# Kernel tuning notes

Hardware: AMD Instinct MI355X
Metric: run time of the kernel (lower is better)

The kernel has to match this reference:

```python
import jax, jax.numpy as jnp
import numpy as np

N = 100000      # nodes
E = 3200000     # directed edges (avg degree 32)
F_IN = 512      # data.num_features
H = 64          # hidden_channels
C = 8           # data.num_classes


def setup_inputs() -> dict:
    key = jax.random.key(0)
    k = jax.random.split(key, 5)
    x = jax.random.normal(k[0], (N, F_IN), dtype=jnp.float32)
    edge_index = jax.random.randint(k[1], (2, E), 0, N, dtype=jnp.int32)
    W1 = jax.random.normal(k[2], (F_IN, H), dtype=jnp.float32) * (1.0 / np.sqrt(F_IN))
    b1 = jnp.zeros((H,), dtype=jnp.float32)
    W2 = jax.random.normal(k[3], (H, C), dtype=jnp.float32) * (1.0 / np.sqrt(H))
    b2 = jnp.zeros((C,), dtype=jnp.float32)
    return {"x": x, "edge_index": edge_index, "W1": W1, "b1": b1, "W2": W2, "b2": b2}


def _gcn_conv(x, W, b, src, dst, n):
    # PyG GCNConv: transform first, then aggregate with symmetric normalization.
    h = x @ W  # [N, out]
    ones = jnp.ones(src.shape[0], dtype=h.dtype)
    deg = jax.ops.segment_sum(ones, dst, num_segments=n)          # in-degree incl. self-loop
    dinv = jnp.where(deg > 0, jax.lax.rsqrt(deg), 0.0)
    norm = dinv[src] * dinv[dst]                                   # [E+N]
    out = jax.ops.segment_sum(h[src] * norm[:, None], dst, num_segments=n)
    return out + b


def reference(x, edge_index, W1, b1, W2, b2):
    # add self-loops once (gcn_norm adds them inside each GCNConv)
    loops = jnp.arange(N, dtype=edge_index.dtype)
    src = jnp.concatenate([edge_index[0], loops])
    dst = jnp.concatenate([edge_index[1], loops])
    h = jax.nn.relu(_gcn_conv(x, W1, b1, src, dst, N))
    # F.dropout(training=False) -> identity in eval mode
    return _gcn_conv(h, W2, b2, src, dst, N)
```

## Files before the change

kernel.cpp:

```cpp
#include <hip/hip_runtime.h>
#include <cstdint>
#include <cstddef>


#define NODE_SHIFT 7
#define NODE_RANGE 128
#define MAX_B 1024
#define CHUNK 16384

__device__ __forceinline__ unsigned short f2bf(float f) {
    unsigned u = __float_as_uint(f);
    u += 0x7FFFu + ((u >> 16) & 1u);
    return (unsigned short)(u >> 16);
}
__device__ __forceinline__ float bf2f(unsigned short h) {
    return __uint_as_float((unsigned)h << 16);
}

__global__ void k_zero(int* __restrict__ p, int n) {
    int i = blockIdx.x * blockDim.x + threadIdx.x;
    if (i < n) p[i] = 0;
}

__global__ __launch_bounds__(256) void k_bcount(const int* __restrict__ dst,
                                                int* __restrict__ bucket_cnt,
                                                int* __restrict__ blk_base,
                                                int E, int B) {
    __shared__ int hist[MAX_B];
    int t = threadIdx.x;
    for (int i = t; i < B; i += 256) hist[i] = 0;
    __syncthreads();
    int base = blockIdx.x * CHUNK;
#pragma unroll 8
    for (int j = 0; j < CHUNK / 256; ++j) {
        int e = base + j * 256 + t;
        if (e < E) atomicAdd(&hist[dst[e] >> NODE_SHIFT], 1);
    }
    __syncthreads();
    for (int i = t; i < B; i += 256)
        blk_base[(size_t)blockIdx.x * B + i] = atomicAdd(&bucket_cnt[i], hist[i]);
}

__global__ __launch_bounds__(1024) void k_bscan(const int* __restrict__ bucket_cnt,
                                                int* __restrict__ bucket_start,
                                                int* __restrict__ rowptr,
                                                int B, int N) {
    __shared__ int s[1024];
    int t = threadIdx.x;
    int v = (t < B) ? bucket_cnt[t] : 0;
    s[t] = v;
    __syncthreads();
    for (int off = 1; off < 1024; off <<= 1) {
        int add = (t >= off) ? s[t - off] : 0;
        __syncthreads();
        s[t] += add;
        __syncthreads();
    }
    if (t < B) bucket_start[t] = s[t] - v;
    if (t == 1023) {
        bucket_start[B] = s[1023];
        rowptr[N] = s[1023];
    }
}

__global__ __launch_bounds__(256) void k_bscatter(const int* __restrict__ src,
                                                  const int* __restrict__ dst,
                                                  const int* __restrict__ bucket_start,
                                                  const int* __restrict__ blk_base,
                                                  unsigned* __restrict__ bucket_pk,
                                                  int E, int B) {
    __shared__ int cur[MAX_B];
    int t = threadIdx.x;
    for (int i = t; i < B; i += 256)
        cur[i] = bucket_start[i] + blk_base[(size_t)blockIdx.x * B + i];
    __syncthreads();
    int base = blockIdx.x * CHUNK;
#pragma unroll 8
    for (int j = 0; j < CHUNK / 256; ++j) {
        int e = base + j * 256 + t;
        if (e < E) {
            int d = dst[e];
            int p = atomicAdd(&cur[d >> NODE_SHIFT], 1);
            bucket_pk[p] = (unsigned)src[e] | ((unsigned)(d & (NODE_RANGE - 1)) << 25);
        }
    }
}

__global__ __launch_bounds__(256) void k_bfinal(const unsigned* __restrict__ bucket_pk,
                                                const int* __restrict__ bucket_start,
                                                int* __restrict__ rowptr,
                                                float* __restrict__ dinv,
                                                int* __restrict__ csr_src,
                                                int N) {
    __shared__ int hist[NODE_RANGE];
    __shared__ int sc[NODE_RANGE];
    int t = threadIdx.x;
    int node0 = blockIdx.x * NODE_RANGE;
    int nn = min(NODE_RANGE, N - node0);
    int estart = bucket_start[blockIdx.x];
    int eend   = bucket_start[blockIdx.x + 1];

    if (t < NODE_RANGE) hist[t] = 0;
    __syncthreads();
    for (int e = estart + t; e < eend; e += 256)
        atomicAdd(&hist[bucket_pk[e] >> 25], 1);
    __syncthreads();

    int v = 0;
    if (t < NODE_RANGE) { v = hist[t]; sc[t] = v; }
    __syncthreads();
    for (int off = 1; off < NODE_RANGE; off <<= 1) {
        int add = (t < NODE_RANGE && t >= off) ? sc[t - off] : 0;
        __syncthreads();
        if (t < NODE_RANGE) sc[t] += add;
        __syncthreads();
    }

    int excl = (t < NODE_RANGE) ? (sc[t] - v) : 0;
    if (t < NODE_RANGE) hist[t] = estart + excl;
    if (t < nn) {
        rowptr[node0 + t] = estart + excl;
        dinv[node0 + t] = rsqrtf((float)(v + 1));
    }
    __syncthreads();

    for (int e = estart + t; e < eend; e += 256) {
        unsigned q = bucket_pk[e];
        int slot = atomicAdd(&hist[q >> 25], 1);
        csr_src[slot] = (int)(q & 0x01FFFFFFu);
    }
}


__global__ __launch_bounds__(256) void k_gemm1(const float* __restrict__ x,
                                               const float* __restrict__ W1,
                                               unsigned short* __restrict__ h1,
                                               int N) {
    __shared__ float xsT[32][68];
    __shared__ float ws[32][64];
    int t = threadIdx.x;
    int tc = t & 15;
    int tr = t >> 4;
    int row0 = blockIdx.x * 64;

    float acc[4][4] = {{0.f}};

    int lr  = t >> 2;
    int lkq = (t & 3) * 8;

    for (int k0 = 0; k0 < 512; k0 += 32) {
        {
            int gr = row0 + lr;
            float4 v0 = {0.f, 0.f, 0.f, 0.f}, v1 = {0.f, 0.f, 0.f, 0.f};
            if (gr < N) {
                const float* p = x + (size_t)gr * 512 + k0 + lkq;
                v0 = *(const float4*)p;
                v1 = *(const float4*)(p + 4);
            }
            xsT[lkq + 0][lr] = v0.x; xsT[lkq + 1][lr] = v0.y;
            xsT[lkq + 2][lr] = v0.z; xsT[lkq + 3][lr] = v0.w;
            xsT[lkq + 4][lr] = v1.x; xsT[lkq + 5][lr] = v1.y;
            xsT[lkq + 6][lr] = v1.z; xsT[lkq + 7][lr] = v1.w;
        }
        {
            const float* p = W1 + (size_t)k0 * 64 + t * 8;
            float4 v0 = *(const float4*)p;
            float4 v1 = *(const float4*)(p + 4);
            int kk = (t * 8) >> 6;
            int cc = (t * 8) & 63;
            *(float4*)&ws[kk][cc]     = v0;
            *(float4*)&ws[kk][cc + 4] = v1;
        }
        __syncthreads();

#pragma unroll
        for (int kk = 0; kk < 32; ++kk) {
            float4 a = *(const float4*)&xsT[kk][tr * 4];
            float4 b = *(const float4*)&ws[kk][tc * 4];
            acc[0][0] += a.x * b.x; acc[0][1] += a.x * b.y;
            acc[0][2] += a.x * b.z; acc[0][3] += a.x * b.w;
            acc[1][0] += a.y * b.x; acc[1][1] += a.y * b.y;
            acc[1][2] += a.y * b.z; acc[1][3] += a.y * b.w;
            acc[2][0] += a.z * b.x; acc[2][1] += a.z * b.y;
            acc[2][2] += a.z * b.z; acc[2][3] += a.z * b.w;
            acc[3][0] += a.w * b.x; acc[3][1] += a.w * b.y;
            acc[3][2] += a.w * b.z; acc[3][3] += a.w * b.w;
        }
        __syncthreads();
    }

#pragma unroll
    for (int r = 0; r < 4; ++r) {
        int gr = row0 + tr * 4 + r;
        if (gr < N) {
            ushort4 o;
            o.x = f2bf(acc[r][0]); o.y = f2bf(acc[r][1]);
            o.z = f2bf(acc[r][2]); o.w = f2bf(acc[r][3]);
            *(ushort4*)&h1[(size_t)gr * 64 + tc * 4] = o;
        }
    }
}


__global__ __launch_bounds__(256) void k_agg1(const unsigned short* __restrict__ h1,
                                              const int* __restrict__ rowptr,
                                              const int* __restrict__ csr_src,
                                              const float* __restrict__ dinv,
                                              const float* __restrict__ b1,
                                              const float* __restrict__ W2,
                                              float* __restrict__ h2, int N) {
    int wid = threadIdx.x >> 6;
    int lane = threadIdx.x & 63;
    int n = blockIdx.x * 4 + wid;
    if (n >= N) return;

    float w2r[8];
#pragma unroll
    for (int c = 0; c < 8; ++c) w2r[c] = W2[lane * 8 + c];
    float bias = b1[lane];
    float dn   = dinv[n];
    float self = bf2f(h1[(size_t)n * 64 + lane]);

    int start = __builtin_amdgcn_readfirstlane(rowptr[n]);
    int cnt   = __builtin_amdgcn_readfirstlane(rowptr[n + 1]) - start;
    const int* qp = csr_src + start;

    float acc0 = 0.f, acc1 = 0.f;
    int i = 0;
    for (; i + 8 <= cnt; i += 8) {
        int q0 = qp[i + 0]; int q1 = qp[i + 1];
        int q2 = qp[i + 2]; int q3 = qp[i + 3];
        int q4 = qp[i + 4]; int q5 = qp[i + 5];
        int q6 = qp[i + 6]; int q7 = qp[i + 7];
        float w0 = dinv[q0]; float w1 = dinv[q1];
        float w2 = dinv[q2]; float w3 = dinv[q3];
        float w4 = dinv[q4]; float w5 = dinv[q5];
        float w6 = dinv[q6]; float w7 = dinv[q7];
        float v0 = bf2f(h1[(size_t)q0 * 64 + lane]);
        float v1 = bf2f(h1[(size_t)q1 * 64 + lane]);
        float v2 = bf2f(h1[(size_t)q2 * 64 + lane]);
        float v3 = bf2f(h1[(size_t)q3 * 64 + lane]);
        float v4 = bf2f(h1[(size_t)q4 * 64 + lane]);
        float v5 = bf2f(h1[(size_t)q5 * 64 + lane]);
        float v6 = bf2f(h1[(size_t)q6 * 64 + lane]);
        float v7 = bf2f(h1[(size_t)q7 * 64 + lane]);
        acc0 = fmaf(w0, v0, acc0);
        acc1 = fmaf(w1, v1, acc1);
        acc0 = fmaf(w2, v2, acc0);
        acc1 = fmaf(w3, v3, acc1);
        acc0 = fmaf(w4, v4, acc0);
        acc1 = fmaf(w5, v5, acc1);
        acc0 = fmaf(w6, v6, acc0);
        acc1 = fmaf(w7, v7, acc1);
    }
    for (; i < cnt; ++i) {
        int q = qp[i];
        acc0 = fmaf(dinv[q], bf2f(h1[(size_t)q * 64 + lane]), acc0);
    }

    float r = fmaxf(dn * ((acc0 + acc1) + dn * self) + bias, 0.f);

    float keep = 0.f;
#pragma unroll
    for (int c = 0; c < 8; ++c) {
        float s = r * w2r[c];
#pragma unroll
        for (int k = 1; k < 64; k <<= 1) s += __shfl_xor(s, k, 64);
        keep = ((lane & 7) == c) ? s : keep;
    }
    if (lane < 8) h2[(size_t)n * 8 + lane] = keep;
}


__global__ __launch_bounds__(256) void k_agg2(const float* __restrict__ h2,
                                              const int* __restrict__ rowptr,
                                              const int* __restrict__ csr_src,
                                              const float* __restrict__ dinv,
                                              const float* __restrict__ b2,
                                              float* __restrict__ out, int N) {
    int wid = threadIdx.x >> 6;
    int lane = threadIdx.x & 63;
    int n = blockIdx.x * 4 + wid;
    if (n >= N) return;
    int start = rowptr[n];
    int cnt = rowptr[n + 1] - start;
    int c = lane & 7;
    int ii = lane >> 3;

    float a0 = 0.f, a1 = 0.f;
    int i = ii;
    for (; i + 8 < cnt; i += 16) {
        int q0 = csr_src[start + i];
        int q1 = csr_src[start + i + 8];
        float w0 = dinv[q0], w1 = dinv[q1];
        float v0 = h2[(size_t)q0 * 8 + c];
        float v1 = h2[(size_t)q1 * 8 + c];
        a0 = fmaf(w0, v0, a0);
        a1 = fmaf(w1, v1, a1);
    }
    if (i < cnt) {
        int q = csr_src[start + i];
        a0 = fmaf(dinv[q], h2[(size_t)q * 8 + c], a0);
    }
    float acc = a0 + a1;
    acc += __shfl_xor(acc, 8, 64);
    acc += __shfl_xor(acc, 16, 64);
    acc += __shfl_xor(acc, 32, 64);

    if (lane < 8) {
        float dn = dinv[n];
        out[(size_t)n * 8 + lane] =
            dn * (acc + dn * h2[(size_t)n * 8 + lane]) + b2[lane];
    }
}


extern "C" void kernel_launch(void* const* d_in, const int* in_sizes, int n_in,
                              void* d_out, int out_size, void* d_ws, size_t ws_size,
                              hipStream_t stream) {
    const float* x  = (const float*)d_in[0];
    const int*   ei = (const int*)d_in[1];
    const float* W1 = (const float*)d_in[2];
    const float* b1 = (const float*)d_in[3];
    const float* W2 = (const float*)d_in[4];
    const float* b2 = (const float*)d_in[5];
    float* out = (float*)d_out;

    const int H   = in_sizes[3];
    const int FIN = in_sizes[2] / H;
    const int N   = in_sizes[0] / FIN;
    const int E   = in_sizes[1] / 2;
    const int* srcA = ei;
    const int* dstA = ei + E;

    const int B    = (N + NODE_RANGE - 1) >> NODE_SHIFT;
    const int nCnt = (E + CHUNK - 1) / CHUNK;

    char* ws = (char*)d_ws;
    size_t off = 0;
    auto alloc = [&](size_t bytes) -> void* {
        void* p = ws + off;
        off += (bytes + 255) & ~(size_t)255;
        return p;
    };
    int*      bucket_cnt   = (int*)alloc((size_t)B * 4);
    int*      bucket_start = (int*)alloc((size_t)(B + 1) * 4);
    int*      blk_base     = (int*)alloc((size_t)nCnt * B * 4);
    unsigned* bucket_pk    = (unsigned*)alloc((size_t)E * 4);
    int*      csr_src      = (int*)alloc((size_t)E * 4);
    int*      rowptr       = (int*)alloc((size_t)(N + 1) * 4);
    float*    dinv         = (float*)alloc((size_t)N * 4);
    unsigned short* h1     = (unsigned short*)alloc((size_t)N * 64 * 2);
    float*    h2           = (float*)alloc((size_t)N * 8 * 4);
    (void)ws_size; (void)n_in; (void)out_size;

    k_zero    <<<(B + 255) / 256, 256, 0, stream>>>(bucket_cnt, B);
    k_bcount  <<<nCnt, 256, 0, stream>>>(dstA, bucket_cnt, blk_base, E, B);
    k_bscan   <<<1, 1024, 0, stream>>>(bucket_cnt, bucket_start, rowptr, B, N);
    k_bscatter<<<nCnt, 256, 0, stream>>>(srcA, dstA, bucket_start, blk_base,
                                         bucket_pk, E, B);
    k_bfinal  <<<B, 256, 0, stream>>>(bucket_pk, bucket_start, rowptr, dinv,
                                      csr_src, N);
    k_gemm1   <<<(N + 63) / 64, 256, 0, stream>>>(x, W1, h1, N);
    k_agg1    <<<(N + 3) / 4, 256, 0, stream>>>(h1, rowptr, csr_src, dinv, b1, W2, h2, N);
    k_agg2    <<<(N + 3) / 4, 256, 0, stream>>>(h2, rowptr, csr_src, dinv, b2, out, N);
}
```

Measured before the change: 598.8 us.

## Use split-bf16 MFMA for first GEMM and vectorize neighbor gathers in agg1

```diff
diff --git a/kernel.cpp b/kernel.cpp
--- a/kernel.cpp
+++ b/kernel.cpp
@@ -7,6 +7,9 @@
 #define NODE_RANGE 128
 #define MAX_B 1024
 #define CHUNK 16384
+
+typedef short short8 __attribute__((ext_vector_type(8)));
+typedef float f32x4 __attribute__((ext_vector_type(4)));
 
 __device__ __forceinline__ unsigned short f2bf(float f) {
     unsigned u = __float_as_uint(f);
@@ -136,69 +139,88 @@
                                                const float* __restrict__ W1,
                                                unsigned short* __restrict__ h1,
                                                int N) {
-    __shared__ float xsT[32][68];
-    __shared__ float ws[32][64];
+    __shared__ unsigned short Ah[128][40];
+    __shared__ unsigned short Al[128][40];
+    __shared__ unsigned short Bh[64][40];
+    __shared__ unsigned short Bl[64][40];
+
     int t = threadIdx.x;
-    int tc = t & 15;
-    int tr = t >> 4;
-    int row0 = blockIdx.x * 64;
-
-    float acc[4][4] = {{0.f}};
-
-    int lr  = t >> 2;
-    int lkq = (t & 3) * 8;
+    int w = t >> 6;
+    int l = t & 63;
+    int row0 = blockIdx.x * 128;
+    int lr = l & 15;
+    int lk = (l >> 4) * 8;
+
+    f32x4 acc[2][4];
+#pragma unroll
+    for (int mb = 0; mb < 2; ++mb)
+#pragma unroll
+        for (int nb = 0; nb < 4; ++nb)
+            acc[mb][nb] = (f32x4){0.f, 0.f, 0.f, 0.f};
 
     for (int k0 = 0; k0 < 512; k0 += 32) {
-        {
-            int gr = row0 + lr;
-            float4 v0 = {0.f, 0.f, 0.f, 0.f}, v1 = {0.f, 0.f, 0.f, 0.f};
-            if (gr < N) {
-                const float* p = x + (size_t)gr * 512 + k0 + lkq;
-                v0 = *(const float4*)p;
-                v1 = *(const float4*)(p + 4);
+#pragma unroll
+        for (int j = 0; j < 4; ++j) {
+            int idx = t + j * 256;
+            int r   = idx >> 3;
+            int c4  = idx & 7;
+            float4 v = {0.f, 0.f, 0.f, 0.f};
+            int gr = row0 + r;
+            if (gr < N) v = *(const float4*)(x + (size_t)gr * 512 + k0 + c4 * 4);
+            ushort4 hi, lo;
+            hi.x = f2bf(v.x); lo.x = f2bf(v.x - bf2f(hi.x));
+            hi.y = f2bf(v.y); lo.y = f2bf(v.y - bf2f(hi.y));
+            hi.z = f2bf(v.z); lo.z = f2bf(v.z - bf2f(hi.z));
+            hi.w = f2bf(v.w); lo.w = f2bf(v.w - bf2f(hi.w));
+            *(ushort4*)&Ah[r][c4 * 4] = hi;
+            *(ushort4*)&Al[r][c4 * 4] = lo;
+        }
+#pragma unroll
+        for (int j = 0; j < 2; ++j) {
+            int idx = t + j * 256;
+            int kk  = idx >> 4;
+            int c4  = idx & 15;
+            float4 v = *(const float4*)(W1 + (size_t)(k0 + kk) * 64 + c4 * 4);
+            unsigned short h, lo2;
+            h = f2bf(v.x); lo2 = f2bf(v.x - bf2f(h));
+            Bh[c4 * 4 + 0][kk] = h; Bl[c4 * 4 + 0][kk] = lo2;
+            h = f2bf(v.y); lo2 = f2bf(v.y - bf2f(h));
+            Bh[c4 * 4 + 1][kk] = h; Bl[c4 * 4 + 1][kk] = lo2;
+            h = f2bf(v.z); lo2 = f2bf(v.z - bf2f(h));
+            Bh[c4 * 4 + 2][kk] = h; Bl[c4 * 4 + 2][kk] = lo2;
+            h = f2bf(v.w); lo2 = f2bf(v.w - bf2f(h));
+            Bh[c4 * 4 + 3][kk] = h; Bl[c4 * 4 + 3][kk] = lo2;
+        }
+        __syncthreads();
+
+        short8 a0h = *(const short8*)&Ah[w * 32 + lr][lk];
+        short8 a0l = *(const short8*)&Al[w * 32 + lr][lk];
+        short8 a1h = *(const short8*)&Ah[w * 32 + 16 + lr][lk];
+        short8 a1l = *(const short8*)&Al[w * 32 + 16 + lr][lk];
+#pragma unroll
+        for (int nb = 0; nb < 4; ++nb) {
+            short8 bh = *(const short8*)&Bh[nb * 16 + lr][lk];
+            short8 bl = *(const short8*)&Bl[nb * 16 + lr][lk];
+            acc[0][nb] = __builtin_amdgcn_mfma_f32_16x16x32_bf16(a0h, bh, acc[0][nb], 0, 0, 0);
+            acc[0][nb] = __builtin_amdgcn_mfma_f32_16x16x32_bf16(a0l, bh, acc[0][nb], 0, 0, 0);
+            acc[0][nb] = __builtin_amdgcn_mfma_f32_16x16x32_bf16(a0h, bl, acc[0][nb], 0, 0, 0);
+            acc[1][nb] = __builtin_amdgcn_mfma_f32_16x16x32_bf16(a1h, bh, acc[1][nb], 0, 0, 0);
+            acc[1][nb] = __builtin_amdgcn_mfma_f32_16x16x32_bf16(a1l, bh, acc[1][nb], 0, 0, 0);
+            acc[1][nb] = __builtin_amdgcn_mfma_f32_16x16x32_bf16(a1h, bl, acc[1][nb], 0, 0, 0);
+        }
+        __syncthreads();
+    }
+
+#pragma unroll
+    for (int mb = 0; mb < 2; ++mb)
+#pragma unroll
+        for (int nb = 0; nb < 4; ++nb)
+#pragma unroll
+            for (int r = 0; r < 4; ++r) {
+                int gr = row0 + w * 32 + mb * 16 + (l >> 4) * 4 + r;
+                int gc = nb * 16 + (l & 15);
+                if (gr < N) h1[(size_t)gr * 64 + gc] = f2bf(acc[mb][nb][r]);
             }
-            xsT[lkq + 0][lr] = v0.x; xsT[lkq + 1][lr] = v0.y;
-            xsT[lkq + 2][lr] = v0.z; xsT[lkq + 3][lr] = v0.w;
-            xsT[lkq + 4][lr] = v1.x; xsT[lkq + 5][lr] = v1.y;
-            xsT[lkq + 6][lr] = v1.z; xsT[lkq + 7][lr] = v1.w;
-        }
-        {
-            const float* p = W1 + (size_t)k0 * 64 + t * 8;
-            float4 v0 = *(const float4*)p;
-            float4 v1 = *(const float4*)(p + 4);
-            int kk = (t * 8) >> 6;
-            int cc = (t * 8) & 63;
-            *(float4*)&ws[kk][cc]     = v0;
-            *(float4*)&ws[kk][cc + 4] = v1;
-        }
-        __syncthreads();
-
-#pragma unroll
-        for (int kk = 0; kk < 32; ++kk) {
-            float4 a = *(const float4*)&xsT[kk][tr * 4];
-            float4 b = *(const float4*)&ws[kk][tc * 4];
-            acc[0][0] += a.x * b.x; acc[0][1] += a.x * b.y;
-            acc[0][2] += a.x * b.z; acc[0][3] += a.x * b.w;
-            acc[1][0] += a.y * b.x; acc[1][1] += a.y * b.y;
-            acc[1][2] += a.y * b.z; acc[1][3] += a.y * b.w;
-            acc[2][0] += a.z * b.x; acc[2][1] += a.z * b.y;
-            acc[2][2] += a.z * b.z; acc[2][3] += a.z * b.w;
-            acc[3][0] += a.w * b.x; acc[3][1] += a.w * b.y;
-            acc[3][2] += a.w * b.z; acc[3][3] += a.w * b.w;
-        }
-        __syncthreads();
-    }
-
-#pragma unroll
-    for (int r = 0; r < 4; ++r) {
-        int gr = row0 + tr * 4 + r;
-        if (gr < N) {
-            ushort4 o;
-            o.x = f2bf(acc[r][0]); o.y = f2bf(acc[r][1]);
-            o.z = f2bf(acc[r][2]); o.w = f2bf(acc[r][3]);
-            *(ushort4*)&h1[(size_t)gr * 64 + tc * 4] = o;
-        }
-    }
 }
 
 
@@ -213,59 +235,90 @@
     int lane = threadIdx.x & 63;
     int n = blockIdx.x * 4 + wid;
     if (n >= N) return;
-
-    float w2r[8];
-#pragma unroll
-    for (int c = 0; c < 8; ++c) w2r[c] = W2[lane * 8 + c];
-    float bias = b1[lane];
-    float dn   = dinv[n];
-    float self = bf2f(h1[(size_t)n * 64 + lane]);
+    int qtr = lane >> 4;
+    int cb  = (lane & 15) * 4;
+
+    float w2r[4][8];
+#pragma unroll
+    for (int j = 0; j < 4; ++j)
+#pragma unroll
+        for (int c = 0; c < 8; ++c) w2r[j][c] = W2[(cb + j) * 8 + c];
+    float4 bias = *(const float4*)(b1 + cb);
+    float dn = dinv[n];
+    ushort4 sv = *(const ushort4*)&h1[(size_t)n * 64 + cb];
 
     int start = __builtin_amdgcn_readfirstlane(rowptr[n]);
     int cnt   = __builtin_amdgcn_readfirstlane(rowptr[n + 1]) - start;
     const int* qp = csr_src + start;
 
-    float acc0 = 0.f, acc1 = 0.f;
+    float ax = 0.f, ay = 0.f, az = 0.f, aw = 0.f;
     int i = 0;
-    for (; i + 8 <= cnt; i += 8) {
-        int q0 = qp[i + 0]; int q1 = qp[i + 1];
-        int q2 = qp[i + 2]; int q3 = qp[i + 3];
-        int q4 = qp[i + 4]; int q5 = qp[i + 5];
-        int q6 = qp[i + 6]; int q7 = qp[i + 7];
-        float w0 = dinv[q0]; float w1 = dinv[q1];
-        float w2 = dinv[q2]; float w3 = dinv[q3];
-        float w4 = dinv[q4]; float w5 = dinv[q5];
-        float w6 = dinv[q6]; float w7 = dinv[q7];
-        float v0 = bf2f(h1[(size_t)q0 * 64 + lane]);
-        float v1 = bf2f(h1[(size_t)q1 * 64 + lane]);
-        float v2 = bf2f(h1[(size_t)q2 * 64 + lane]);
-        float v3 = bf2f(h1[(size_t)q3 * 64 + lane]);
-        float v4 = bf2f(h1[(size_t)q4 * 64 + lane]);
-        float v5 = bf2f(h1[(size_t)q5 * 64 + lane]);
-        float v6 = bf2f(h1[(size_t)q6 * 64 + lane]);
-        float v7 = bf2f(h1[(size_t)q7 * 64 + lane]);
-        acc0 = fmaf(w0, v0, acc0);
-        acc1 = fmaf(w1, v1, acc1);
-        acc0 = fmaf(w2, v2, acc0);
-        acc1 = fmaf(w3, v3, acc1);
-        acc0 = fmaf(w4, v4, acc0);
-        acc1 = fmaf(w5, v5, acc1);
-        acc0 = fmaf(w6, v6, acc0);
-        acc1 = fmaf(w7, v7, acc1);
-    }
-    for (; i < cnt; ++i) {
-        int q = qp[i];
-        acc0 = fmaf(dinv[q], bf2f(h1[(size_t)q * 64 + lane]), acc0);
-    }
-
-    float r = fmaxf(dn * ((acc0 + acc1) + dn * self) + bias, 0.f);
+    for (; i + 16 <= cnt; i += 16) {
+        int q0 = qp[i      + qtr];
+        int q1 = qp[i + 4  + qtr];
+        int q2 = qp[i + 8  + qtr];
+        int q3 = qp[i + 12 + qtr];
+        float w0 = dinv[q0], w1 = dinv[q1], w2 = dinv[q2], w3 = dinv[q3];
+        ushort4 v0 = *(const ushort4*)&h1[(size_t)q0 * 64 + cb];
+        ushort4 v1 = *(const ushort4*)&h1[(size_t)q1 * 64 + cb];
+        ushort4 v2 = *(const ushort4*)&h1[(size_t)q2 * 64 + cb];
+        ushort4 v3 = *(const ushort4*)&h1[(size_t)q3 * 64 + cb];
+        ax = fmaf(w0, bf2f(v0.x), ax); ay = fmaf(w0, bf2f(v0.y), ay);
+        az = fmaf(w0, bf2f(v0.z), az); aw = fmaf(w0, bf2f(v0.w), aw);
+        ax = fmaf(w1, bf2f(v1.x), ax); ay = fmaf(w1, bf2f(v1.y), ay);
+        az = fmaf(w1, bf2f(v1.z), az); aw = fmaf(w1, bf2f(v1.w), aw);
+        ax = fmaf(w2, bf2f(v2.x), ax); ay = fmaf(w2, bf2f(v2.y), ay);
+        az = fmaf(w2, bf2f(v2.z), az); aw = fmaf(w2, bf2f(v2.w), aw);
+        ax = fmaf(w3, bf2f(v3.x), ax); ay = fmaf(w3, bf2f(v3.y), ay);
+        az = fmaf(w3, bf2f(v3.z), az); aw = fmaf(w3, bf2f(v3.w), aw);
+    }
+    if (i + 8 <= cnt) {
+        int q0 = qp[i + qtr];
+        int q1 = qp[i + 4 + qtr];
+        float w0 = dinv[q0], w1 = dinv[q1];
+        ushort4 v0 = *(const ushort4*)&h1[(size_t)q0 * 64 + cb];
+        ushort4 v1 = *(const ushort4*)&h1[(size_t)q1 * 64 + cb];
+        ax = fmaf(w0, bf2f(v0.x), ax); ay = fmaf(w0, bf2f(v0.y), ay);
+        az = fmaf(w0, bf2f(v0.z), az); aw = fmaf(w0, bf2f(v0.w), aw);
+        ax = fmaf(w1, bf2f(v1.x), ax); ay = fmaf(w1, bf2f(v1.y), ay);
+        az = fmaf(w1, bf2f(v1.z), az); aw = fmaf(w1, bf2f(v1.w), aw);
+        i += 8;
+    }
+    if (i + 4 <= cnt) {
+        int q0 = qp[i + qtr];
+        float w0 = dinv[q0];
+        ushort4 v0 = *(const ushort4*)&h1[(size_t)q0 * 64 + cb];
+        ax = fmaf(w0, bf2f(v0.x), ax); ay = fmaf(w0, bf2f(v0.y), ay);
+        az = fmaf(w0, bf2f(v0.z), az); aw = fmaf(w0, bf2f(v0.w), aw);
+        i += 4;
+    }
+    int rem = cnt - i;
+    if (qtr < rem) {
+        int q0 = qp[i + qtr];
+        float w0 = dinv[q0];
+        ushort4 v0 = *(const ushort4*)&h1[(size_t)q0 * 64 + cb];
+        ax = fmaf(w0, bf2f(v0.x), ax); ay = fmaf(w0, bf2f(v0.y), ay);
+        az = fmaf(w0, bf2f(v0.z), az); aw = fmaf(w0, bf2f(v0.w), aw);
+    }
+
+    ax += __shfl_xor(ax, 16, 64); ax += __shfl_xor(ax, 32, 64);
+    ay += __shfl_xor(ay, 16, 64); ay += __shfl_xor(ay, 32, 64);
+    az += __shfl_xor(az, 16, 64); az += __shfl_xor(az, 32, 64);
+    aw += __shfl_xor(aw, 16, 64); aw += __shfl_xor(aw, 32, 64);
+
+    float r0 = fmaxf(dn * (ax + dn * bf2f(sv.x)) + bias.x, 0.f);
+    float r1 = fmaxf(dn * (ay + dn * bf2f(sv.y)) + bias.y, 0.f);
+    float r2 = fmaxf(dn * (az + dn * bf2f(sv.z)) + bias.z, 0.f);
+    float r3 = fmaxf(dn * (aw + dn * bf2f(sv.w)) + bias.w, 0.f);
 
     float keep = 0.f;
 #pragma unroll
     for (int c = 0; c < 8; ++c) {
-        float s = r * w2r[c];
-#pragma unroll
-        for (int k = 1; k < 64; k <<= 1) s += __shfl_xor(s, k, 64);
+        float s = r0 * w2r[0][c] + r1 * w2r[1][c] + r2 * w2r[2][c] + r3 * w2r[3][c];
+        s += __shfl_xor(s, 1, 64);
+        s += __shfl_xor(s, 2, 64);
+        s += __shfl_xor(s, 4, 64);
+        s += __shfl_xor(s, 8, 64);
         keep = ((lane & 7) == c) ? s : keep;
     }
     if (lane < 8) h2[(size_t)n * 8 + lane] = keep;
@@ -361,7 +414,7 @@
                                          bucket_pk, E, B);
     k_bfinal  <<<B, 256, 0, stream>>>(bucket_pk, bucket_start, rowptr, dinv,
                                       csr_src, N);
-    k_gemm1   <<<(N + 63) / 64, 256, 0, stream>>>(x, W1, h1, N);
+    k_gemm1   <<<(N + 127) / 128, 256, 0, stream>>>(x, W1, h1, N);
     k_agg1    <<<(N + 3) / 4, 256, 0, stream>>>(h1, rowptr, csr_src, dinv, b1, W2, h2, N);
     k_agg2    <<<(N + 3) / 4, 256, 0, stream>>>(h2, rowptr, csr_src, dinv, b2, out, N);
 }
```

After: 656.1 us. 9.6% more time.
